# Performance work log

Hardware: AMD Instinct MI355X
Metric: run time of the kernel (lower is better)

The kernel has to match this reference:

```python
import jax, jax.numpy as jnp
import numpy as np

NUM_EDGE_TYPES = 8
NUM_NODE_TYPES = 3


def _rgcn_conv(x, edge_index, edge_type, node_type, rel_W, root_W, root_b):
    """One RGCNConv layer: per-relation mean aggregation + per-node-type root transform.
    x: [N, din]; rel_W: [R, din, dout]; root_W: [T, din, dout]; root_b: [T, dout]."""
    src, dst = edge_index[0], edge_index[1]
    N = x.shape[0]
    dout = rel_W.shape[-1]
    xs = x[src]  # [E, din] gather once, reused by all relations
    out = jnp.zeros((N, dout), dtype=x.dtype)
    for r in range(rel_W.shape[0]):
        w = (edge_type == r).astype(x.dtype)  # [E] relation mask
        msg = (xs @ rel_W[r]) * w[:, None]    # [E, dout]
        s = jax.ops.segment_sum(msg, dst, num_segments=N)   # [N, dout]
        cnt = jax.ops.segment_sum(w, dst, num_segments=N)   # [N]
        out = out + jnp.where(cnt[:, None] > 0, s / jnp.maximum(cnt, 1.0)[:, None], 0.0)
    for t in range(root_W.shape[0]):
        m = (node_type == t).astype(x.dtype)[:, None]
        out = out + m * (x @ root_W[t] + root_b[t])
    return out


def _group_input(x0, x1, emb2, node_type, local_node_idx):
    # h[n] = x_{node_type[n]}[local_node_idx[n]]
    g0 = x0[local_node_idx]
    g1 = x1[local_node_idx]
    g2 = emb2[local_node_idx]
    nt = node_type[:, None]
    return jnp.where(nt == 0, g0, jnp.where(nt == 1, g1, g2))


def setup_inputs() -> dict:
    key = jax.random.key(0)
    ks = jax.random.split(key, 16)
    N_PER_TYPE, D_IN, D_H, D_OUT = 40000, 128, 128, 349
    N = 3 * N_PER_TYPE
    E = 1920000
    s_in = 1.0 / np.sqrt(D_IN)
    inp = {
        "x0": jax.random.normal(ks[0], (N_PER_TYPE, D_IN), jnp.float32),
        "x1": jax.random.normal(ks[1], (N_PER_TYPE, D_IN), jnp.float32),
        "emb2": jax.random.normal(ks[2], (N_PER_TYPE, D_IN), jnp.float32),
        "rel_W1": jax.random.normal(ks[3], (NUM_EDGE_TYPES, D_IN, D_H), jnp.float32) * s_in,
        "root_W1": jax.random.normal(ks[4], (NUM_NODE_TYPES, D_IN, D_H), jnp.float32) * s_in,
        "root_b1": jax.random.normal(ks[5], (NUM_NODE_TYPES, D_H), jnp.float32) * 0.01,
        "rel_W2": jax.random.normal(ks[6], (NUM_EDGE_TYPES, D_H, D_OUT), jnp.float32) * s_in,
        "root_W2": jax.random.normal(ks[7], (NUM_NODE_TYPES, D_H, D_OUT), jnp.float32) * s_in,
        "root_b2": jax.random.normal(ks[8], (NUM_NODE_TYPES, D_OUT), jnp.float32) * 0.01,
        "edge_index": jax.random.randint(ks[9], (2, E), 0, N, jnp.int64),
        "edge_type": jax.random.randint(ks[10], (E,), 0, NUM_EDGE_TYPES, jnp.int64),
        "node_type": jax.random.randint(ks[11], (N,), 0, NUM_NODE_TYPES, jnp.int64),
        "local_node_idx": jax.random.randint(ks[12], (N,), 0, N_PER_TYPE, jnp.int64),
    }
    return inp


def reference(x0, x1, emb2, rel_W1, root_W1, root_b1, rel_W2, root_W2, root_b2,
              edge_index, edge_type, node_type, local_node_idx):
    x = _group_input(x0, x1, emb2, node_type, local_node_idx)          # [N, D_IN]
    x = _rgcn_conv(x, edge_index, edge_type, node_type, rel_W1, root_W1, root_b1)
    x = jax.nn.relu(x)  # dropout is identity in eval mode
    x = _rgcn_conv(x, edge_index, edge_type, node_type, rel_W2, root_W2, root_b2)
    return jax.nn.log_softmax(x, axis=-1)
```

## Files before the change

kernel.cpp:

```cpp
#include <hip/hip_runtime.h>

#define DH 128
#define KTOT 1408
#define LDA 40
#define DOUT2 349
#define DOUT2P 384

typedef short v8s __attribute__((ext_vector_type(8)));
typedef float v4f __attribute__((ext_vector_type(4)));

__device__ __forceinline__ unsigned short f2bf(float f) {
  unsigned int u = __float_as_uint(f);
  u += 0x7fffu + ((u >> 16) & 1u);
  return (unsigned short)(u >> 16);
}
__device__ __forceinline__ unsigned int pack2(float a, float b) {
  return (unsigned int)f2bf(a) | ((unsigned int)f2bf(b) << 16);
}

__global__ void k_detect(const int* __restrict__ nt_raw, int* __restrict__ flag, int half) {
  int i = blockIdx.x * 256 + threadIdx.x;
  if (i >= half) return;
  if (nt_raw[2 * i + 1] != 0) atomicOr(flag, 1);
}
__global__ void k_cvt(const int* __restrict__ in, int* __restrict__ out, int n,
                      const int* __restrict__ flag) {
  int i = blockIdx.x * 256 + threadIdx.x;
  if (i >= n) return;
  out[i] = (*flag) ? in[i] : in[2 * i];
}

__global__ void k_gather(const float4* __restrict__ x0, const float4* __restrict__ x1,
                         const float4* __restrict__ x2, const int* __restrict__ nt,
                         const int* __restrict__ li, ushort4* __restrict__ xout, int total) {
  int i = blockIdx.x * 256 + threadIdx.x;
  if (i >= total) return;
  int node = i >> 5, c = i & 31;
  int t = nt[node];
  int l = li[node];
  const float4* s = (t == 0) ? x0 : (t == 1) ? x1 : x2;
  float4 v = s[(size_t)l * 32 + c];
  ushort4 o;
  o.x = f2bf(v.x); o.y = f2bf(v.y); o.z = f2bf(v.z); o.w = f2bf(v.w);
  xout[i] = o;
}

__global__ void k_count(const int* __restrict__ src_dst, const int* __restrict__ et,
                        int* __restrict__ cnt, int E) {
  int i = blockIdx.x * 256 + threadIdx.x;
  if (i >= E) return;
  int dst = src_dst[E + i];
  int r = et[i];
  atomicAdd(&cnt[dst * 8 + r], 1);
}

__global__ __launch_bounds__(1024) void k_scan1(const int* __restrict__ cnt,
                                                int* __restrict__ outl,
                                                int* __restrict__ bsums, int n) {
  __shared__ int s[1024];
  int tid = threadIdx.x;
  int gid = blockIdx.x * 1024 + tid;
  int v = (gid < n) ? cnt[gid] : 0;
  s[tid] = v;
  __syncthreads();
  for (int o = 1; o < 1024; o <<= 1) {
    int t = (tid >= o) ? s[tid - o] : 0;
    __syncthreads();
    s[tid] += t;
    __syncthreads();
  }
  if (gid < n) outl[gid] = s[tid] - v;
  if (tid == 1023) bsums[blockIdx.x] = s[1023];
}
__global__ __launch_bounds__(1024) void k_scan2(int* __restrict__ bsums, int nb) {
  __shared__ int s[1024];
  int tid = threadIdx.x;
  int v = (tid < nb) ? bsums[tid] : 0;
  s[tid] = v;
  __syncthreads();
  for (int o = 1; o < 1024; o <<= 1) {
    int t = (tid >= o) ? s[tid - o] : 0;
    __syncthreads();
    s[tid] += t;
    __syncthreads();
  }
  if (tid < nb) bsums[tid] = s[tid] - v;
}
__global__ __launch_bounds__(1024) void k_scan3(int* __restrict__ offs,
                                                const int* __restrict__ bsums, int n, int total) {
  int gid = blockIdx.x * 1024 + threadIdx.x;
  if (gid < n) offs[gid] += bsums[blockIdx.x];
  if (gid == 0) offs[n] = total;
}

__global__ void k_scatter(const int* __restrict__ src_dst, const int* __restrict__ et,
                          int* __restrict__ cur, int* __restrict__ srcs, int E) {
  int i = blockIdx.x * 256 + threadIdx.x;
  if (i >= E) return;
  int dst = src_dst[E + i];
  int r = et[i];
  int pos = atomicAdd(&cur[dst * 8 + r], 1);
  srcs[pos] = src_dst[i];
}

__global__ void k_prepw(const float* __restrict__ rel,
                        const float* __restrict__ root,
                        unsigned short* __restrict__ Wt, int dout, int doutp) {
  int i = blockIdx.x * 256 + threadIdx.x;
  int tot = doutp * KTOT;
  if (i >= tot) return;
  int n = i / KTOT;
  int k = i - n * KTOT;
  unsigned short v = 0;
  if (n < dout)
    v = f2bf((k < 1024) ? rel[(size_t)k * dout + n] : root[(size_t)(k - 1024) * dout + n]);
  Wt[i] = v;
}

__global__ __launch_bounds__(256) void k_aggregate(const unsigned int* __restrict__ xin,
                                                   unsigned int* __restrict__ yout,
                                                   const int* __restrict__ offs,
                                                   const int* __restrict__ srcs,
                                                   const int* __restrict__ node_type,
                                                   int m0, int mc) {
  int wl = blockIdx.x * 4 + (threadIdx.x >> 6);
  if (wl >= mc) return;
  int w = m0 + wl;
  int lane = threadIdx.x & 63;
  unsigned int* yrow = yout + (size_t)wl * 704;
  int base = w * 8;
#pragma unroll 1
  for (int r = 0; r < 8; ++r) {
    int s = offs[base + r], e = offs[base + r + 1];
    float a0 = 0.f, a1 = 0.f;
    for (int j = s; j < e; ++j) {
      int src = srcs[j];
      unsigned int u = xin[(size_t)src * 64 + lane];
      a0 += __uint_as_float(u << 16);
      a1 += __uint_as_float(u & 0xffff0000u);
    }
    int c = e - s;
    float sc = (c > 0) ? 1.0f / (float)c : 0.0f;
    yrow[r * 64 + lane] = pack2(a0 * sc, a1 * sc);
  }
  unsigned int uself = xin[(size_t)w * 64 + lane];
  int nt = node_type[w];
#pragma unroll
  for (int t = 0; t < 3; ++t) yrow[(8 + t) * 64 + lane] = (nt == t) ? uself : 0u;
}

__global__ __launch_bounds__(256) void k_gemm(const unsigned short* __restrict__ Y,
                                              const unsigned short* __restrict__ Wt,
                                              const int* __restrict__ node_type,
                                              const float* __restrict__ bias,
                                              unsigned short* __restrict__ outH,
                                              float* __restrict__ outF,
                                              int M, int dout, int mode) {
  __shared__ unsigned short Al[128 * LDA];
  __shared__ unsigned short Bl[128 * LDA];
  int tid = threadIdx.x;
  int m0 = blockIdx.x * 128;
  int n0 = blockIdx.y * 128;
  int lane = tid & 63;
  int w = tid >> 6;
  int wm = (w >> 1) * 64, wn = (w & 1) * 64;
  int l15 = lane & 15, q = lane >> 4;

  v4f acc[4][4];
#pragma unroll
  for (int i = 0; i < 4; ++i)
#pragma unroll
    for (int j = 0; j < 4; ++j) acc[i][j] = (v4f){0.f, 0.f, 0.f, 0.f};

  int arow = tid >> 2, aseg = tid & 3;

  for (int k0 = 0; k0 < KTOT; k0 += 32) {
#pragma unroll
    for (int rr = 0; rr < 128; rr += 64) {
      int row = arow + rr;
      int gm = m0 + row;
      uint4 av = {0u, 0u, 0u, 0u};
      if (gm < M) av = *(const uint4*)(Y + (size_t)gm * KTOT + k0 + aseg * 8);
      *(uint4*)(Al + row * LDA + aseg * 8) = av;
      uint4 bv = *(const uint4*)(Wt + (size_t)(n0 + row) * KTOT + k0 + aseg * 8);
      *(uint4*)(Bl + row * LDA + aseg * 8) = bv;
    }
    __syncthreads();
    v8s a[4], b[4];
#pragma unroll
    for (int ti = 0; ti < 4; ++ti)
      a[ti] = *(const v8s*)(Al + (wm + ti * 16 + l15) * LDA + q * 8);
#pragma unroll
    for (int tj = 0; tj < 4; ++tj)
      b[tj] = *(const v8s*)(Bl + (wn + tj * 16 + l15) * LDA + q * 8);
#pragma unroll
    for (int ti = 0; ti < 4; ++ti)
#pragma unroll
      for (int tj = 0; tj < 4; ++tj)
        acc[ti][tj] = __builtin_amdgcn_mfma_f32_16x16x32_bf16(a[ti], b[tj], acc[ti][tj], 0, 0, 0);
    __syncthreads();
  }

#pragma unroll
  for (int ti = 0; ti < 4; ++ti) {
#pragma unroll
    for (int i = 0; i < 4; ++i) {
      int row = m0 + wm + ti * 16 + q * 4 + i;
      if (row >= M) continue;
      int nt = node_type[row];
      const float* brow = bias + nt * dout;
#pragma unroll
      for (int tj = 0; tj < 4; ++tj) {
        int col = n0 + wn + tj * 16 + l15;
        if (col >= dout) continue;
        float v = acc[ti][tj][i] + brow[col];
        if (mode == 1) {
          v = v > 0.f ? v : 0.f;
          outH[(size_t)row * dout + col] = f2bf(v);
        } else {
          outF[(size_t)row * dout + col] = v;
        }
      }
    }
  }
}

__global__ __launch_bounds__(256) void k_softmax(float* __restrict__ X, int M) {
  int w = blockIdx.x * 4 + (threadIdx.x >> 6);
  if (w >= M) return;
  int lane = threadIdx.x & 63;
  float* row = X + (size_t)w * DOUT2;
  float v[6];
  float mx = -3.0e38f;
#pragma unroll
  for (int i = 0; i < 6; ++i) {
    int c = lane + i * 64;
    v[i] = (c < DOUT2) ? row[c] : -3.0e38f;
    mx = fmaxf(mx, v[i]);
  }
#pragma unroll
  for (int o = 32; o > 0; o >>= 1) mx = fmaxf(mx, __shfl_xor(mx, o));
  float s = 0.f;
#pragma unroll
  for (int i = 0; i < 6; ++i) {
    int c = lane + i * 64;
    if (c < DOUT2) s += __expf(v[i] - mx);
  }
#pragma unroll
  for (int o = 32; o > 0; o >>= 1) s += __shfl_xor(s, o);
  float ls = __logf(s);
#pragma unroll
  for (int i = 0; i < 6; ++i) {
    int c = lane + i * 64;
    if (c < DOUT2) row[c] = v[i] - mx - ls;
  }
}

extern "C" void kernel_launch(void* const* d_in, const int* in_sizes, int n_in,
                              void* d_out, int out_size, void* d_ws, size_t ws_size,
                              hipStream_t stream) {
  const float* x0 = (const float*)d_in[0];
  const float* x1 = (const float*)d_in[1];
  const float* emb2 = (const float*)d_in[2];
  const float* relW1 = (const float*)d_in[3];
  const float* rootW1 = (const float*)d_in[4];
  const float* rootb1 = (const float*)d_in[5];
  const float* relW2 = (const float*)d_in[6];
  const float* rootW2 = (const float*)d_in[7];
  const float* rootb2 = (const float*)d_in[8];
  const int* ei_raw = (const int*)d_in[9];
  const int* et_raw = (const int*)d_in[10];
  const int* nt_raw = (const int*)d_in[11];
  const int* li_raw = (const int*)d_in[12];

  const int E = in_sizes[10];
  const int N = in_sizes[11];
  const int NK = N * 8;

  char* p = (char*)d_ws;
  auto alloc = [&](size_t bytes) {
    char* r = p;
    p += (bytes + 255) & ~(size_t)255;
    return r;
  };
  unsigned short* xbuf = (unsigned short*)alloc((size_t)N * DH * 2);
  unsigned short* hbuf = (unsigned short*)alloc((size_t)N * DH * 2);
  unsigned short* wt1 = (unsigned short*)alloc((size_t)128 * KTOT * 2);
  unsigned short* wt2 = (unsigned short*)alloc((size_t)DOUT2P * KTOT * 2);
  int* offs = (int*)alloc((size_t)(NK + 1) * 4);
  int* cur = (int*)alloc((size_t)NK * 4);
  int* srcs = (int*)alloc((size_t)E * 4);
  int* bsums = (int*)alloc(4096);
  int* ei32 = (int*)alloc((size_t)2 * E * 4);
  int* et32 = (int*)alloc((size_t)E * 4);
  int* nt32 = (int*)alloc((size_t)N * 4);
  int* li32 = (int*)alloc((size_t)N * 4);
  int* flag = (int*)alloc(256);

  size_t used = (size_t)(p - (char*)d_ws);
  size_t avail = (ws_size > used) ? (ws_size - used) : 0;
  long long maxRows = (long long)(avail / ((size_t)KTOT * 2));
  int chunk = (int)((maxRows / 128) * 128);
  int Nceil = ((N + 127) / 128) * 128;
  if (chunk > Nceil) chunk = Nceil;
  if (chunk < 128) chunk = 128;
  unsigned short* ych = (unsigned short*)p;

  float* outF = (float*)d_out;
  const int nScanBlocks = (NK + 1023) / 1024;

  hipMemsetAsync(flag, 0, 4, stream);
  hipMemsetAsync(cur, 0, (size_t)NK * 4, stream);
  k_detect<<<(N / 2 + 255) / 256, 256, 0, stream>>>(nt_raw, flag, N / 2);
  k_cvt<<<(2 * E + 255) / 256, 256, 0, stream>>>(ei_raw, ei32, 2 * E, flag);
  k_cvt<<<(E + 255) / 256, 256, 0, stream>>>(et_raw, et32, E, flag);
  k_cvt<<<(N + 255) / 256, 256, 0, stream>>>(nt_raw, nt32, N, flag);
  k_cvt<<<(N + 255) / 256, 256, 0, stream>>>(li_raw, li32, N, flag);

  k_gather<<<(N * 32 + 255) / 256, 256, 0, stream>>>((const float4*)x0, (const float4*)x1,
                                                     (const float4*)emb2, nt32, li32,
                                                     (ushort4*)xbuf, N * 32);
  k_count<<<(E + 255) / 256, 256, 0, stream>>>(ei32, et32, cur, E);
  k_scan1<<<nScanBlocks, 1024, 0, stream>>>(cur, offs, bsums, NK);
  k_scan2<<<1, 1024, 0, stream>>>(bsums, nScanBlocks);
  k_scan3<<<nScanBlocks, 1024, 0, stream>>>(offs, bsums, NK, E);
  hipMemcpyAsync(cur, offs, (size_t)NK * 4, hipMemcpyDeviceToDevice, stream);
  k_scatter<<<(E + 255) / 256, 256, 0, stream>>>(ei32, et32, cur, srcs, E);
  k_prepw<<<(128 * KTOT + 255) / 256, 256, 0, stream>>>(relW1, rootW1, wt1, 128, 128);
  k_prepw<<<(DOUT2P * KTOT + 255) / 256, 256, 0, stream>>>(relW2, rootW2, wt2, DOUT2, DOUT2P);
  for (int m0 = 0; m0 < N; m0 += chunk) {
    int mc = (N - m0 < chunk) ? (N - m0) : chunk;
    k_aggregate<<<(mc + 3) / 4, 256, 0, stream>>>((const unsigned int*)xbuf, (unsigned int*)ych,
                                                  offs, srcs, nt32, m0, mc);
    dim3 g1((mc + 127) / 128, 1);
    k_gemm<<<g1, 256, 0, stream>>>(ych, wt1, nt32 + m0, rootb1, hbuf + (size_t)m0 * DH,
                                   (float*)nullptr, mc, 128, 1);
  }
  for (int m0 = 0; m0 < N; m0 += chunk) {
    int mc = (N - m0 < chunk) ? (N - m0) : chunk;
    k_aggregate<<<(mc + 3) / 4, 256, 0, stream>>>((const unsigned int*)hbuf, (unsigned int*)ych,
                                                  offs, srcs, nt32, m0, mc);
    dim3 g2((mc + 127) / 128, DOUT2P / 128);
    k_gemm<<<g2, 256, 0, stream>>>(ych, wt2, nt32 + m0, rootb2, (unsigned short*)nullptr,
                                   outF + (size_t)m0 * DOUT2, mc, DOUT2, 2);
  }
  k_softmax<<<(N + 3) / 4, 256, 0, stream>>>(outF, N);
}
```

Baseline: 1.591 ms.

## Split aggregation across two waves per node and use direct global-to-LDS loads in GEMM

The aggregation kernel now gives each destination node two wavefronts, each handling four relations, and unrolls the edge loop by two with separate accumulators to keep more gathers in flight. The GEMM replaces register-staged tile loads with global_load_lds direct-to-LDS transfers on an unpadded 32-wide layout. It also swaps the grid axes so N tiles vary fastest and share the A tile in cache. The row bound check on A loads is dropped, so the last chunk may read past M rows. The unpadded LDS layout may also cause bank conflicts.

```diff
diff --git a/kernel.cpp b/kernel.cpp
--- a/kernel.cpp
+++ b/kernel.cpp
@@ -2,7 +2,6 @@
 
 #define DH 128
 #define KTOT 1408
-#define LDA 40
 #define DOUT2 349
 #define DOUT2P 384
 
@@ -16,6 +15,11 @@
 }
 __device__ __forceinline__ unsigned int pack2(float a, float b) {
   return (unsigned int)f2bf(a) | ((unsigned int)f2bf(b) << 16);
+}
+
+__device__ __forceinline__ void gl2lds16(const unsigned short* g, unsigned short* l) {
+  __builtin_amdgcn_global_load_lds((const __attribute__((address_space(1))) unsigned int*)g,
+                                   (__attribute__((address_space(3))) unsigned int*)l, 16, 0, 0);
 }
 
 __global__ void k_detect(const int* __restrict__ nt_raw, int* __restrict__ flag, int half) {
@@ -123,30 +127,44 @@
                                                    const int* __restrict__ srcs,
                                                    const int* __restrict__ node_type,
                                                    int m0, int mc) {
-  int wl = blockIdx.x * 4 + (threadIdx.x >> 6);
+  int wid = blockIdx.x * 4 + (threadIdx.x >> 6);
+  int wl = wid >> 1;
+  int h = wid & 1;
   if (wl >= mc) return;
   int w = m0 + wl;
   int lane = threadIdx.x & 63;
   unsigned int* yrow = yout + (size_t)wl * 704;
-  int base = w * 8;
-#pragma unroll 1
-  for (int r = 0; r < 8; ++r) {
+  int base = w * 8 + h * 4;
+#pragma unroll
+  for (int r = 0; r < 4; ++r) {
     int s = offs[base + r], e = offs[base + r + 1];
-    float a0 = 0.f, a1 = 0.f;
-    for (int j = s; j < e; ++j) {
-      int src = srcs[j];
-      unsigned int u = xin[(size_t)src * 64 + lane];
-      a0 += __uint_as_float(u << 16);
-      a1 += __uint_as_float(u & 0xffff0000u);
+    float a0 = 0.f, a1 = 0.f, b0 = 0.f, b1 = 0.f;
+    int j = s;
+    for (; j + 2 <= e; j += 2) {
+      int s1 = srcs[j], s2 = srcs[j + 1];
+      unsigned int u1 = xin[(size_t)s1 * 64 + lane];
+      unsigned int u2 = xin[(size_t)s2 * 64 + lane];
+      a0 += __uint_as_float(u1 << 16);
+      a1 += __uint_as_float(u1 & 0xffff0000u);
+      b0 += __uint_as_float(u2 << 16);
+      b1 += __uint_as_float(u2 & 0xffff0000u);
+    }
+    if (j < e) {
+      int s1 = srcs[j];
+      unsigned int u1 = xin[(size_t)s1 * 64 + lane];
+      a0 += __uint_as_float(u1 << 16);
+      a1 += __uint_as_float(u1 & 0xffff0000u);
     }
     int c = e - s;
     float sc = (c > 0) ? 1.0f / (float)c : 0.0f;
-    yrow[r * 64 + lane] = pack2(a0 * sc, a1 * sc);
-  }
-  unsigned int uself = xin[(size_t)w * 64 + lane];
-  int nt = node_type[w];
-#pragma unroll
-  for (int t = 0; t < 3; ++t) yrow[(8 + t) * 64 + lane] = (nt == t) ? uself : 0u;
+    yrow[(h * 4 + r) * 64 + lane] = pack2((a0 + b0) * sc, (a1 + b1) * sc);
+  }
+  if (h == 0) {
+    unsigned int uself = xin[(size_t)w * 64 + lane];
+    int nt = node_type[w];
+#pragma unroll
+    for (int t = 0; t < 3; ++t) yrow[(8 + t) * 64 + lane] = (nt == t) ? uself : 0u;
+  }
 }
 
 __global__ __launch_bounds__(256) void k_gemm(const unsigned short* __restrict__ Y,
@@ -156,11 +174,11 @@
                                               unsigned short* __restrict__ outH,
                                               float* __restrict__ outF,
                                               int M, int dout, int mode) {
-  __shared__ unsigned short Al[128 * LDA];
-  __shared__ unsigned short Bl[128 * LDA];
+  __shared__ unsigned short Al[128 * 32];
+  __shared__ unsigned short Bl[128 * 32];
   int tid = threadIdx.x;
-  int m0 = blockIdx.x * 128;
-  int n0 = blockIdx.y * 128;
+  int n0 = blockIdx.x * 128;
+  int m0 = blockIdx.y * 128;
   int lane = tid & 63;
   int w = tid >> 6;
   int wm = (w >> 1) * 64, wn = (w & 1) * 64;
@@ -172,27 +190,25 @@
 #pragma unroll
     for (int j = 0; j < 4; ++j) acc[i][j] = (v4f){0.f, 0.f, 0.f, 0.f};
 
-  int arow = tid >> 2, aseg = tid & 3;
+  int rbase = 16 * (2 * w);
+  const unsigned short* Ag0 = Y + (size_t)(m0 + rbase + (lane >> 2)) * KTOT + 8 * (lane & 3);
+  const unsigned short* Bg0 = Wt + (size_t)(n0 + rbase + (lane >> 2)) * KTOT + 8 * (lane & 3);
+  unsigned short* Asl0 = Al + (2 * w) * 512;
+  unsigned short* Bsl0 = Bl + (2 * w) * 512;
 
   for (int k0 = 0; k0 < KTOT; k0 += 32) {
-#pragma unroll
-    for (int rr = 0; rr < 128; rr += 64) {
-      int row = arow + rr;
-      int gm = m0 + row;
-      uint4 av = {0u, 0u, 0u, 0u};
-      if (gm < M) av = *(const uint4*)(Y + (size_t)gm * KTOT + k0 + aseg * 8);
-      *(uint4*)(Al + row * LDA + aseg * 8) = av;
-      uint4 bv = *(const uint4*)(Wt + (size_t)(n0 + row) * KTOT + k0 + aseg * 8);
-      *(uint4*)(Bl + row * LDA + aseg * 8) = bv;
-    }
+    gl2lds16(Ag0 + k0, Asl0);
+    gl2lds16(Ag0 + (size_t)16 * KTOT + k0, Asl0 + 512);
+    gl2lds16(Bg0 + k0, Bsl0);
+    gl2lds16(Bg0 + (size_t)16 * KTOT + k0, Bsl0 + 512);
     __syncthreads();
     v8s a[4], b[4];
 #pragma unroll
     for (int ti = 0; ti < 4; ++ti)
-      a[ti] = *(const v8s*)(Al + (wm + ti * 16 + l15) * LDA + q * 8);
+      a[ti] = *(const v8s*)(Al + (wm + ti * 16 + l15) * 32 + q * 8);
 #pragma unroll
     for (int tj = 0; tj < 4; ++tj)
-      b[tj] = *(const v8s*)(Bl + (wn + tj * 16 + l15) * LDA + q * 8);
+      b[tj] = *(const v8s*)(Bl + (wn + tj * 16 + l15) * 32 + q * 8);
 #pragma unroll
     for (int ti = 0; ti < 4; ++ti)
 #pragma unroll
@@ -330,17 +346,17 @@
   k_prepw<<<(DOUT2P * KTOT + 255) / 256, 256, 0, stream>>>(relW2, rootW2, wt2, DOUT2, DOUT2P);
   for (int m0 = 0; m0 < N; m0 += chunk) {
     int mc = (N - m0 < chunk) ? (N - m0) : chunk;
-    k_aggregate<<<(mc + 3) / 4, 256, 0, stream>>>((const unsigned int*)xbuf, (unsigned int*)ych,
-                                                  offs, srcs, nt32, m0, mc);
-    dim3 g1((mc + 127) / 128, 1);
+    k_aggregate<<<(2 * mc + 3) / 4, 256, 0, stream>>>((const unsigned int*)xbuf,
+                                                      (unsigned int*)ych, offs, srcs, nt32, m0, mc);
+    dim3 g1(1, (mc + 127) / 128);
     k_gemm<<<g1, 256, 0, stream>>>(ych, wt1, nt32 + m0, rootb1, hbuf + (size_t)m0 * DH,
                                    (float*)nullptr, mc, 128, 1);
   }
   for (int m0 = 0; m0 < N; m0 += chunk) {
     int mc = (N - m0 < chunk) ? (N - m0) : chunk;
-    k_aggregate<<<(mc + 3) / 4, 256, 0, stream>>>((const unsigned int*)hbuf, (unsigned int*)ych,
-                                                  offs, srcs, nt32, m0, mc);
-    dim3 g2((mc + 127) / 128, DOUT2P / 128);
+    k_aggregate<<<(2 * mc + 3) / 4, 256, 0, stream>>>((const unsigned int*)hbuf,
+                                                      (unsigned int*)ych, offs, srcs, nt32, m0, mc);
+    dim3 g2(DOUT2P / 128, (mc + 127) / 128);
     k_gemm<<<g2, 256, 0, stream>>>(ych, wt2, nt32 + m0, rootb2, (unsigned short*)nullptr,
                                    outF + (size_t)m0 * DOUT2, mc, DOUT2, 2);
   }
```

Result: faster. 1.356 ms (-14.8%).
